# Kernel optimization log

Measured on AMD Instinct MI355X. Metric: run time of the kernel, lower is better.

The kernel has to match this reference:

```python
import jax, jax.numpy as jnp
import numpy as np

MS_KS = 9
C = 256
BN_EPS = 1e-5


def setup_inputs() -> dict:
    key = jax.random.key(0)
    k1, k2, k3 = jax.random.split(key, 3)
    p2_r = jax.random.normal(k1, (2, C, 64, 128), dtype=jnp.float32)
    conv_w = jax.random.normal(k2, (C, C, 1, MS_KS), dtype=jnp.float32) * 0.02
    conv1_w = jax.random.normal(k3, (1, C, 1, 1), dtype=jnp.float32) * 0.05
    bn_gamma = jnp.ones((1,), jnp.float32)
    bn_beta = jnp.zeros((1,), jnp.float32)
    return dict(p2_r=p2_r, conv_w=conv_w, conv1_w=conv1_w,
                bn_gamma=bn_gamma, bn_beta=bn_beta)


def _scnn_pass(x, M):
    # x: [b,c,h,w]. Each step applies conv(1,ms_ks) to a width-1 column with
    # zero padding ms_ks//2 -> only the center tap contributes, i.e. a 256x256
    # channel matmul per column, followed by relu and residual add.
    cols = jnp.moveaxis(x, 3, 0)  # [w,b,c,h]
    def step(carry, col):
        new = col + jax.nn.relu(jnp.einsum('oc,bch->boh', M, carry))
        return new, new
    _, outs = jax.lax.scan(step, cols[0], cols[1:])
    outs = jnp.concatenate([cols[:1], outs], axis=0)[::-1]  # mirrors out[::-1]
    return jnp.moveaxis(outs, 0, 3)


def _upsample_bilinear_ac(x, factor=4):
    # F.interpolate(mode='bilinear', align_corners=True)
    b, c, h, w = x.shape
    Ho, Wo = factor * h, factor * w
    ys = jnp.arange(Ho, dtype=x.dtype) * ((h - 1) / (Ho - 1))
    xs = jnp.arange(Wo, dtype=x.dtype) * ((w - 1) / (Wo - 1))
    y0 = jnp.floor(ys).astype(jnp.int32)
    y1 = jnp.minimum(y0 + 1, h - 1)
    wy = (ys - y0.astype(x.dtype))[None, None, :, None]
    rows = x[:, :, y0, :] * (1 - wy) + x[:, :, y1, :] * wy  # [b,c,Ho,w]
    x0 = jnp.floor(xs).astype(jnp.int32)
    x1 = jnp.minimum(x0 + 1, w - 1)
    wx = (xs - x0.astype(x.dtype))[None, None, None, :]
    return rows[:, :, :, x0] * (1 - wx) + rows[:, :, :, x1] * wx


def reference(p2_r, conv_w, conv1_w, bn_gamma, bn_beta):
    M = conv_w[:, :, 0, MS_KS // 2]  # center tap, [c_out, c_in]
    x = _scnn_pass(p2_r, M)                     # reverse=False
    x = _scnn_pass(x[:, :, :, ::-1], M)         # reverse=True (slices[::-1])
    x = _upsample_bilinear_ac(x, 4)             # [b,256,4h,4w]
    x = jnp.einsum('oc,bchw->bohw', conv1_w[:, :, 0, 0], x)  # 1x1 conv -> 1 ch
    # BatchNorm2d(1), training-mode batch statistics (biased variance)
    mean = jnp.mean(x, axis=(0, 2, 3), keepdims=True)
    var = jnp.mean((x - mean) ** 2, axis=(0, 2, 3), keepdims=True)
    x = (x - mean) * jax.lax.rsqrt(var + BN_EPS)
    x = x * bn_gamma[None, :, None, None] + bn_beta[None, :, None, None]
    return jax.nn.sigmoid(x)
```

## Files before the change

### kernel.cpp

```cpp
#include <hip/hip_runtime.h>


typedef _Float16 f16x8 __attribute__((ext_vector_type(8)));
typedef _Float16 f16x4 __attribute__((ext_vector_type(4)));
typedef float    f32x4 __attribute__((ext_vector_type(4)));

static __device__ __forceinline__ void sync_lds() {
  asm volatile("s_waitcnt lgkmcnt(0)" ::: "memory");
  __builtin_amdgcn_s_barrier();
  asm volatile("" ::: "memory");
}

static __device__ __forceinline__ float dpp_even(float v) {
  int t = __builtin_bit_cast(int, v);
  t = __builtin_amdgcn_update_dpp(t, t, 0xA0, 0xF, 0xF, false);
  return __builtin_bit_cast(float, t);
}

extern "C" __global__ void k_extract(const float* __restrict__ convw,
                                     _Float16* __restrict__ Md) {
  int q = blockIdx.x * 256 + threadIdx.x;
  float4 v = ((const float4*)convw)[q];
  float vv[4] = {v.x, v.y, v.z, v.w};
  int f = q * 4;
#pragma unroll
  for (int e = 0; e < 4; ++e) {
    int flat = f + e;
    if (flat % 9 == 4) Md[flat / 9] = (_Float16)vv[e];
  }
}

struct SM {
  _Float16 cy[2][256];
  _Float16 pad_[32];
  _Float16 zh[128 * 256];
};

extern "C" __global__ void __launch_bounds__(512, 2)
k_scan(const float* __restrict__ p2, const _Float16* __restrict__ Md,
       const float* __restrict__ conv1, float* __restrict__ sout,
       float* __restrict__ stats) {
  __shared__ SM sm;
  const int tid  = threadIdx.x;
  const int l    = tid & 63;
  const int r    = tid >> 6;
  const int col  = l & 15;
  const int quad = l >> 4;
  const int b    = blockIdx.x >> 6;
  const int h    = blockIdx.x & 63;

  if (blockIdx.x == 0 && tid == 0) { stats[0] = 0.f; stats[1] = 0.f; }

  const bool isY   = (col == 0);
  const bool isZ   = (col == 1);
  const bool zlane = (l & 1);

  const int m0 = (r * 2 + 0) * 16 + quad * 4;
  const int m1 = (r * 2 + 1) * 16 + quad * 4;

  f16x8 A0[8], A1[8];
#pragma unroll
  for (int ch = 0; ch < 8; ++ch) {
    A0[ch] = *(const f16x8*)(Md + ((r*2+0)*16 + col) * 256 + ch*32 + quad*8);
    A1[ch] = *(const f16x8*)(Md + ((r*2+1)*16 + col) * 256 + ch*32 + quad*8);
  }

  const float* pbase = p2 + (size_t)b * 2097152 + (size_t)h * 128;

  if (isY) {
    float c0a[4], c0b[4];
#pragma unroll
    for (int i = 0; i < 4; ++i) {
      c0a[i] = pbase[(size_t)(m0 + i) * 8192];
      c0b[i] = pbase[(size_t)(m1 + i) * 8192];
    }
    f16x4 pa, pb;
#pragma unroll
    for (int i = 0; i < 4; ++i) { pa[i] = (_Float16)c0a[i]; pb[i] = (_Float16)c0b[i]; }
    *(f16x4*)(sm.cy[0] + m0) = pa; *(f16x4*)(sm.cy[0] + m1) = pb;
    *(f16x4*)(sm.zh    + m0) = pa; *(f16x4*)(sm.zh    + m1) = pb;
  }

  float cca[4], ccb[4], cna[4], cnb[4];
  if (isY) {
#pragma unroll
    for (int i = 0; i < 4; ++i) {
      cca[i] = pbase[(size_t)(m0 + i) * 8192 + 1];
      ccb[i] = pbase[(size_t)(m1 + i) * 8192 + 1];
      cna[i] = pbase[(size_t)(m0 + i) * 8192 + 2];
      cnb[i] = pbase[(size_t)(m1 + i) * 8192 + 2];
    }
  }
  sync_lds();

  const _Float16* pY0 = sm.cy[0] + quad * 8;
  const _Float16* pY1 = sm.cy[1] + quad * 8;
  const _Float16* zrd = sm.zh + quad * 8;
  _Float16*       zwr = sm.zh + 256;

#define STEP(W, PY, WY, CA, CB)                                                \
  do {                                                                         \
    const _Float16* bsrc = zlane ? zrd : (PY);                                 \
    f16x8 B[8];                                                                \
    _Pragma("unroll")                                                          \
    for (int ch = 0; ch < 8; ++ch)                                             \
      B[ch] = *(const f16x8*)(bsrc + ch * 32);                                 \
    f32x4 a00 = {0.f,0.f,0.f,0.f}, a01 = {0.f,0.f,0.f,0.f};                    \
    f32x4 a10 = {0.f,0.f,0.f,0.f}, a11 = {0.f,0.f,0.f,0.f};                    \
    _Pragma("unroll")                                                          \
    for (int ch = 0; ch < 4; ++ch) {                                           \
      a00 = __builtin_amdgcn_mfma_f32_16x16x32_f16(A0[ch],   B[ch],   a00,0,0,0);\
      a10 = __builtin_amdgcn_mfma_f32_16x16x32_f16(A1[ch],   B[ch],   a10,0,0,0);\
      a01 = __builtin_amdgcn_mfma_f32_16x16x32_f16(A0[ch+4], B[ch+4], a01,0,0,0);\
      a11 = __builtin_amdgcn_mfma_f32_16x16x32_f16(A1[ch+4], B[ch+4], a11,0,0,0);\
    }                                                                          \
    f32x4 acc0 = a00 + a01, acc1 = a10 + a11;                                  \
    f32x4 yf0 = {}, yf1 = {};                                                  \
    if (isY) {                                                                 \
      f16x4 yh0, yh1;                                                          \
      _Pragma("unroll")                                                        \
      for (int i = 0; i < 4; ++i) {                                            \
        yf0[i] = (CA)[i] + fmaxf(acc0[i], 0.f);                                \
        yf1[i] = (CB)[i] + fmaxf(acc1[i], 0.f);                                \
        yh0[i] = (_Float16)yf0[i]; yh1[i] = (_Float16)yf1[i];                  \
      }                                                                        \
      *(f16x4*)((WY) + m0) = yh0;                                              \
      *(f16x4*)((WY) + m1) = yh1;                                              \
      if ((W) + 2 < 128) {                                                     \
        _Pragma("unroll")                                                      \
        for (int i = 0; i < 4; ++i) {                                          \
          (CA)[i] = pbase[(size_t)(m0 + i) * 8192 + (W) + 2];                  \
          (CB)[i] = pbase[(size_t)(m1 + i) * 8192 + (W) + 2];                  \
        }                                                                      \
      }                                                                        \
    }                                                                          \
    _Pragma("unroll")                                                          \
    for (int i = 0; i < 4; ++i) {                                              \
      yf0[i] = dpp_even(yf0[i]);                                               \
      yf1[i] = dpp_even(yf1[i]);                                               \
    }                                                                          \
    if (isZ) {                                                                 \
      f16x4 zh0, zh1;                                                          \
      _Pragma("unroll")                                                        \
      for (int i = 0; i < 4; ++i) {                                            \
        zh0[i] = (_Float16)(yf0[i] + fmaxf(acc0[i], 0.f));                     \
        zh1[i] = (_Float16)(yf1[i] + fmaxf(acc1[i], 0.f));                     \
      }                                                                        \
      *(f16x4*)(zwr + m0) = zh0;                                               \
      *(f16x4*)(zwr + m1) = zh1;                                               \
    }                                                                          \
    zrd += 256; zwr += 256;                                                    \
    sync_lds();                                                                \
  } while (0)

#pragma unroll 1
  for (int w = 1; w < 127; w += 2) {
    STEP(w,     pY0, sm.cy[1], cca, ccb);
    STEP(w + 1, pY1, sm.cy[0], cna, cnb);
  }
  STEP(127, pY0, sm.cy[1], cca, ccb);
#undef STEP

  {
    const int w    = tid >> 2;
    const int part = tid & 3;
    const _Float16* zr = sm.zh + w * 256 + part * 64;
    const float*    vr = conv1 + part * 64;
    float s = 0.f;
#pragma unroll
    for (int j = 0; j < 8; ++j) {
      f16x8 zv = *(const f16x8*)(zr + j * 8);
      float4 v0 = *(const float4*)(vr + j * 8);
      float4 v1 = *(const float4*)(vr + j * 8 + 4);
      s += v0.x * (float)zv[0] + v0.y * (float)zv[1]
         + v0.z * (float)zv[2] + v0.w * (float)zv[3]
         + v1.x * (float)zv[4] + v1.y * (float)zv[5]
         + v1.z * (float)zv[6] + v1.w * (float)zv[7];
    }
    s += __shfl_xor(s, 1, 64);
    s += __shfl_xor(s, 2, 64);
    if (part == 0) sout[(blockIdx.x << 7) + (127 - w)] = s;
  }
}

static __device__ __forceinline__ float bilin(const float* __restrict__ s,
                                              int idx) {
  int bb  = idx >> 17;
  int rem = idx & 131071;
  int ho  = rem >> 9;
  int wo  = rem & 511;
  const float SY = 63.0f / 255.0f, SX = 127.0f / 511.0f;
  float fy = (float)ho * SY;
  int y0 = (int)fy; int y1 = min(y0 + 1, 63); float wy = fy - (float)y0;
  float fx = (float)wo * SX;
  int x0 = (int)fx; int x1 = min(x0 + 1, 127); float wx = fx - (float)x0;
  const float* sb = s + bb * 8192;
  float cA = sb[y0 * 128 + x0] * (1.f - wy) + sb[y1 * 128 + x0] * wy;
  float cB = sb[y0 * 128 + x1] * (1.f - wy) + sb[y1 * 128 + x1] * wy;
  return cA * (1.f - wx) + cB * wx;
}

extern "C" __global__ void k_stats(const float* __restrict__ s,
                                   float* __restrict__ stats) {
  int tid  = threadIdx.x;
  int base = blockIdx.x * 1024 + tid;
  float sum = 0.f, ssq = 0.f;
#pragma unroll
  for (int i = 0; i < 4; ++i) {
    float u = bilin(s, base + i * 256);
    sum += u; ssq += u * u;
  }
#pragma unroll
  for (int off = 32; off > 0; off >>= 1) {
    sum += __shfl_xor(sum, off, 64);
    ssq += __shfl_xor(ssq, off, 64);
  }
  __shared__ float ls[4], lq[4];
  int wv = tid >> 6;
  if ((tid & 63) == 0) { ls[wv] = sum; lq[wv] = ssq; }
  __syncthreads();
  if (tid == 0) {
    atomicAdd(&stats[0], ls[0] + ls[1] + ls[2] + ls[3]);
    atomicAdd(&stats[1], lq[0] + lq[1] + lq[2] + lq[3]);
  }
}

extern "C" __global__ void k_norm(const float* __restrict__ s,
                                  const float* __restrict__ stats,
                                  const float* __restrict__ gamma,
                                  const float* __restrict__ beta,
                                  float* __restrict__ out) {
  int tid  = threadIdx.x;
  int base = blockIdx.x * 1024 + tid;
  const float invN = 1.f / 262144.f;
  float mean  = stats[0] * invN;
  float var   = stats[1] * invN - mean * mean;
  float scale = rsqrtf(var + 1e-5f) * gamma[0];
  float bias  = beta[0] - mean * scale;
#pragma unroll
  for (int i = 0; i < 4; ++i) {
    int idx = base + i * 256;
    float u = bilin(s, idx);
    float x = u * scale + bias;
    out[idx] = 1.f / (1.f + __expf(-x));
  }
}

extern "C" void kernel_launch(void* const* d_in, const int* in_sizes, int n_in,
                              void* d_out, int out_size, void* d_ws, size_t ws_size,
                              hipStream_t stream) {
  const float* p2    = (const float*)d_in[0];
  const float* convw = (const float*)d_in[1];
  const float* conv1 = (const float*)d_in[2];
  const float* gamma = (const float*)d_in[3];
  const float* beta  = (const float*)d_in[4];
  float* out = (float*)d_out;

  char* ws = (char*)d_ws;
  float*    s     = (float*)ws;
  float*    stats = (float*)(ws + 65536);
  _Float16* Md    = (_Float16*)(ws + 65792);

  hipLaunchKernelGGL(k_extract, dim3(576), dim3(256), 0, stream, convw, Md);
  hipLaunchKernelGGL(k_scan,    dim3(128), dim3(512), 0, stream, p2, Md, conv1, s, stats);
  hipLaunchKernelGGL(k_stats,   dim3(256), dim3(256), 0, stream, s, stats);
  hipLaunchKernelGGL(k_norm,    dim3(256), dim3(256), 0, stream, s, stats, gamma, beta, out);
}
```

Measured before the change: 178.9 us.

## Batch p2 column prefetch as float4 and fuse stats+norm via grid barrier

The scan kernel now loads the next input columns four at a time as float4, double-buffered, in place of scalar per-step loads, which cuts global load instructions and their latency on the serial recurrence. Launch bounds drop to one block per SM, giving the compiler more registers. The stats and normalize kernels are merged into one kernel that keeps the bilinear values in registers and waits on an atomic counter spin barrier, saving a launch and a recomputation. The spin barrier depends on all 256 blocks being resident at once, and the counter is reset inside k_scan.

```diff
diff --git a/kernel.cpp b/kernel.cpp
--- a/kernel.cpp
+++ b/kernel.cpp
@@ -36,7 +36,7 @@
   _Float16 zh[128 * 256];
 };
 
-extern "C" __global__ void __launch_bounds__(512, 2)
+extern "C" __global__ void __launch_bounds__(512, 1)
 k_scan(const float* __restrict__ p2, const _Float16* __restrict__ Md,
        const float* __restrict__ conv1, float* __restrict__ sout,
        float* __restrict__ stats) {
@@ -49,7 +49,9 @@
   const int b    = blockIdx.x >> 6;
   const int h    = blockIdx.x & 63;
 
-  if (blockIdx.x == 0 && tid == 0) { stats[0] = 0.f; stats[1] = 0.f; }
+  if (blockIdx.x == 0 && tid == 0) {
+    stats[0] = 0.f; stats[1] = 0.f; ((int*)stats)[2] = 0;
+  }
 
   const bool isY   = (col == 0);
   const bool isZ   = (col == 1);
@@ -67,29 +69,25 @@
 
   const float* pbase = p2 + (size_t)b * 2097152 + (size_t)h * 128;
 
+  float4 pA[4], pB[4], qA[4], qB[4];
   if (isY) {
-    float c0a[4], c0b[4];
 #pragma unroll
     for (int i = 0; i < 4; ++i) {
-      c0a[i] = pbase[(size_t)(m0 + i) * 8192];
-      c0b[i] = pbase[(size_t)(m1 + i) * 8192];
+      pA[i] = *(const float4*)(pbase + (size_t)(m0 + i) * 8192);
+      pB[i] = *(const float4*)(pbase + (size_t)(m1 + i) * 8192);
+      qA[i] = *(const float4*)(pbase + (size_t)(m0 + i) * 8192 + 4);
+      qB[i] = *(const float4*)(pbase + (size_t)(m1 + i) * 8192 + 4);
     }
+  }
+
+  if (isY) {
     f16x4 pa, pb;
 #pragma unroll
-    for (int i = 0; i < 4; ++i) { pa[i] = (_Float16)c0a[i]; pb[i] = (_Float16)c0b[i]; }
+    for (int i = 0; i < 4; ++i) {
+      pa[i] = (_Float16)pA[i].x; pb[i] = (_Float16)pB[i].x;
+    }
     *(f16x4*)(sm.cy[0] + m0) = pa; *(f16x4*)(sm.cy[0] + m1) = pb;
     *(f16x4*)(sm.zh    + m0) = pa; *(f16x4*)(sm.zh    + m1) = pb;
-  }
-
-  float cca[4], ccb[4], cna[4], cnb[4];
-  if (isY) {
-#pragma unroll
-    for (int i = 0; i < 4; ++i) {
-      cca[i] = pbase[(size_t)(m0 + i) * 8192 + 1];
-      ccb[i] = pbase[(size_t)(m1 + i) * 8192 + 1];
-      cna[i] = pbase[(size_t)(m0 + i) * 8192 + 2];
-      cnb[i] = pbase[(size_t)(m1 + i) * 8192 + 2];
-    }
   }
   sync_lds();
 
@@ -98,7 +96,7 @@
   const _Float16* zrd = sm.zh + quad * 8;
   _Float16*       zwr = sm.zh + 256;
 
-#define STEP(W, PY, WY, CA, CB)                                                \
+#define STEP(PY, WY, CA, CB, COMP)                                             \
   do {                                                                         \
     const _Float16* bsrc = zlane ? zrd : (PY);                                 \
     f16x8 B[8];                                                                \
@@ -120,19 +118,12 @@
       f16x4 yh0, yh1;                                                          \
       _Pragma("unroll")                                                        \
       for (int i = 0; i < 4; ++i) {                                            \
-        yf0[i] = (CA)[i] + fmaxf(acc0[i], 0.f);                                \
-        yf1[i] = (CB)[i] + fmaxf(acc1[i], 0.f);                                \
+        yf0[i] = (CA)[i].COMP + fmaxf(acc0[i], 0.f);                           \
+        yf1[i] = (CB)[i].COMP + fmaxf(acc1[i], 0.f);                           \
         yh0[i] = (_Float16)yf0[i]; yh1[i] = (_Float16)yf1[i];                  \
       }                                                                        \
       *(f16x4*)((WY) + m0) = yh0;                                              \
       *(f16x4*)((WY) + m1) = yh1;                                              \
-      if ((W) + 2 < 128) {                                                     \
-        _Pragma("unroll")                                                      \
-        for (int i = 0; i < 4; ++i) {                                          \
-          (CA)[i] = pbase[(size_t)(m0 + i) * 8192 + (W) + 2];                  \
-          (CB)[i] = pbase[(size_t)(m1 + i) * 8192 + (W) + 2];                  \
-        }                                                                      \
-      }                                                                        \
     }                                                                          \
     _Pragma("unroll")                                                          \
     for (int i = 0; i < 4; ++i) {                                              \
@@ -153,13 +144,45 @@
     sync_lds();                                                                \
   } while (0)
 
+#define REFILL(SA, SB, W0)                                                     \
+  do {                                                                         \
+    if (isY) {                                                                 \
+      int wt = (W0) <= 124 ? (W0) : 124;                                       \
+      _Pragma("unroll")                                                        \
+      for (int i = 0; i < 4; ++i) {                                            \
+        SA[i] = *(const float4*)(pbase + (size_t)(m0 + i) * 8192 + wt);        \
+        SB[i] = *(const float4*)(pbase + (size_t)(m1 + i) * 8192 + wt);        \
+      }                                                                        \
+    }                                                                          \
+  } while (0)
+
+  STEP(pY0, sm.cy[1], pA, pB, y);
+  STEP(pY1, sm.cy[0], pA, pB, z);
+  STEP(pY0, sm.cy[1], pA, pB, w);
+  REFILL(pA, pB, 8);
+
+  int w0 = 4;
 #pragma unroll 1
-  for (int w = 1; w < 127; w += 2) {
-    STEP(w,     pY0, sm.cy[1], cca, ccb);
-    STEP(w + 1, pY1, sm.cy[0], cna, cnb);
-  }
-  STEP(127, pY0, sm.cy[1], cca, ccb);
+  for (int it = 0; it < 15; ++it) {
+    STEP(pY1, sm.cy[0], qA, qB, x);
+    STEP(pY0, sm.cy[1], qA, qB, y);
+    STEP(pY1, sm.cy[0], qA, qB, z);
+    STEP(pY0, sm.cy[1], qA, qB, w);
+    REFILL(qA, qB, w0 + 8);
+    STEP(pY1, sm.cy[0], pA, pB, x);
+    STEP(pY0, sm.cy[1], pA, pB, y);
+    STEP(pY1, sm.cy[0], pA, pB, z);
+    STEP(pY0, sm.cy[1], pA, pB, w);
+    REFILL(pA, pB, w0 + 12);
+    w0 += 8;
+  }
+
+  STEP(pY1, sm.cy[0], qA, qB, x);
+  STEP(pY0, sm.cy[1], qA, qB, y);
+  STEP(pY1, sm.cy[0], qA, qB, z);
+  STEP(pY0, sm.cy[1], qA, qB, w);
 #undef STEP
+#undef REFILL
 
   {
     const int w    = tid >> 2;
@@ -200,15 +223,19 @@
   return cA * (1.f - wx) + cB * wx;
 }
 
-extern "C" __global__ void k_stats(const float* __restrict__ s,
-                                   float* __restrict__ stats) {
+extern "C" __global__ void k_statsnorm(const float* __restrict__ s,
+                                       float* __restrict__ stats,
+                                       const float* __restrict__ gamma,
+                                       const float* __restrict__ beta,
+                                       float* __restrict__ out) {
   int tid  = threadIdx.x;
   int base = blockIdx.x * 1024 + tid;
+  float u[4];
   float sum = 0.f, ssq = 0.f;
 #pragma unroll
   for (int i = 0; i < 4; ++i) {
-    float u = bilin(s, base + i * 256);
-    sum += u; ssq += u * u;
+    u[i] = bilin(s, base + i * 256);
+    sum += u[i]; ssq += u[i] * u[i];
   }
 #pragma unroll
   for (int off = 32; off > 0; off >>= 1) {
@@ -219,19 +246,17 @@
   int wv = tid >> 6;
   if ((tid & 63) == 0) { ls[wv] = sum; lq[wv] = ssq; }
   __syncthreads();
+  int* cnt = (int*)stats + 2;
   if (tid == 0) {
     atomicAdd(&stats[0], ls[0] + ls[1] + ls[2] + ls[3]);
     atomicAdd(&stats[1], lq[0] + lq[1] + lq[2] + lq[3]);
-  }
-}
-
-extern "C" __global__ void k_norm(const float* __restrict__ s,
-                                  const float* __restrict__ stats,
-                                  const float* __restrict__ gamma,
-                                  const float* __restrict__ beta,
-                                  float* __restrict__ out) {
-  int tid  = threadIdx.x;
-  int base = blockIdx.x * 1024 + tid;
+    __threadfence();
+    atomicAdd(cnt, 1);
+  }
+  volatile int* vc = cnt;
+  while (*vc < 256) { __builtin_amdgcn_s_sleep(8); }
+  __threadfence();
+
   const float invN = 1.f / 262144.f;
   float mean  = stats[0] * invN;
   float var   = stats[1] * invN - mean * mean;
@@ -239,10 +264,8 @@
   float bias  = beta[0] - mean * scale;
 #pragma unroll
   for (int i = 0; i < 4; ++i) {
-    int idx = base + i * 256;
-    float u = bilin(s, idx);
-    float x = u * scale + bias;
-    out[idx] = 1.f / (1.f + __expf(-x));
+    float x = u[i] * scale + bias;
+    out[base + i * 256] = 1.f / (1.f + __expf(-x));
   }
 }
 
@@ -261,8 +284,7 @@
   float*    stats = (float*)(ws + 65536);
   _Float16* Md    = (_Float16*)(ws + 65792);
 
-  hipLaunchKernelGGL(k_extract, dim3(576), dim3(256), 0, stream, convw, Md);
-  hipLaunchKernelGGL(k_scan,    dim3(128), dim3(512), 0, stream, p2, Md, conv1, s, stats);
-  hipLaunchKernelGGL(k_stats,   dim3(256), dim3(256), 0, stream, s, stats);
-  hipLaunchKernelGGL(k_norm,    dim3(256), dim3(256), 0, stream, s, stats, gamma, beta, out);
-}
+  hipLaunchKernelGGL(k_extract,   dim3(576), dim3(256), 0, stream, convw, Md);
+  hipLaunchKernelGGL(k_scan,      dim3(128), dim3(512), 0, stream, p2, Md, conv1, s, stats);
+  hipLaunchKernelGGL(k_statsnorm, dim3(256), dim3(256), 0, stream, s, stats, gamma, beta, out);
+}
```

Result: slower. 220.5 us (+23.3%).
